# Performance work log

Hardware: AMD Instinct MI355X
Metric: run time of the kernel (lower is better)

## Reference

```python
import jax, jax.numpy as jnp
import numpy as np

IMAGE_SIZE = 512
N_ANGLES = 180
BATCH = 1


def setup_inputs() -> dict:
    key = jax.random.key(0)
    sinogram = jax.random.normal(key, (BATCH, N_ANGLES, IMAGE_SIZE), dtype=jnp.float32)
    angles = jnp.arange(N_ANGLES, dtype=jnp.float32)  # degrees, 0..179
    return {"sinogram": sinogram, "angles": angles}


def reference(sinogram, angles):
    # sinogram: [B, N, W]; returns [B, 1, H, W] with H == W == image_size.
    B, N, W = sinogram.shape
    H = W
    th = jnp.deg2rad(angles)
    c, s = jnp.cos(th)[:, None, None], jnp.sin(th)[:, None, None]  # [N,1,1]

    # affine_grid base coords (align_corners=True): linspace(-1, 1, size)
    xs = jnp.linspace(-1.0, 1.0, W)[None, None, :]  # [1,1,W]
    ys = jnp.linspace(-1.0, 1.0, H)[None, :, None]  # [1,H,1]

    # rotation: grid_x = c*x + s*y ; grid_y = -s*x + c*y   -> [N,H,W]
    gx = c * xs + s * ys
    gy = -s * xs + c * ys

    # unnormalize (align_corners=True)
    ix = (gx + 1.0) * 0.5 * (W - 1)
    iy = (gy + 1.0) * 0.5 * (H - 1)

    # bilinear corners in x (the input value only depends on the x index,
    # since the projection is expanded identically along H)
    x0 = jnp.floor(ix)
    x1 = x0 + 1.0
    wx1 = ix - x0
    wx0 = 1.0 - wx1
    mx0 = ((x0 >= 0) & (x0 <= W - 1)).astype(sinogram.dtype)
    mx1 = ((x1 >= 0) & (x1 <= W - 1)).astype(sinogram.dtype)
    x0i = jnp.clip(x0, 0, W - 1).astype(jnp.int32)
    x1i = jnp.clip(x1, 0, W - 1).astype(jnp.int32)

    # y contributes only a (zero-padding-masked) weight
    y0 = jnp.floor(iy)
    y1 = y0 + 1.0
    wy1 = iy - y0
    wy0 = 1.0 - wy1
    my0 = ((y0 >= 0) & (y0 <= H - 1)).astype(sinogram.dtype)
    my1 = ((y1 >= 0) & (y1 <= H - 1)).astype(sinogram.dtype)
    yw = wy0 * my0 + wy1 * my1  # [N,H,W]

    n_idx = jnp.arange(N)[:, None, None]  # [N,1,1]
    g0 = sinogram[:, n_idx, x0i]  # [B,N,H,W]
    g1 = sinogram[:, n_idx, x1i]  # [B,N,H,W]

    val = (wx0 * mx0 * g0 + wx1 * mx1 * g1) * yw  # [B,N,H,W]
    recon = jnp.sum(val, axis=1, keepdims=True) / N  # [B,1,H,W]
    return recon
```

## Files before the change

kernel.cpp:

```cpp
#include <hip/hip_runtime.h>
#include <hip/hip_bf16.h>
#include <math.h>


#define IRD_W 512
#define IRD_N 180
#define WIN   32
#define QN    45
#define IRD_STEP (2.0f / 511.0f)

__global__ __launch_bounds__(1024, 8) void iradon_tile4_kernel(
    const float* __restrict__ sino,
    const float* __restrict__ angles,
    float* __restrict__ out)
{
    __shared__ float4 s_c[IRD_N];
    __shared__ int2   s_base[IRD_N];
    __shared__ float  s_win[IRD_N][2 * WIN];
    __shared__ float  s_redA[3][256];
    __shared__ float  s_redB[3][256];

    const int tid = threadIdx.x;
    const int x0 = (blockIdx.x & 31) << 4;
    const int y0 = (blockIdx.x >> 5) << 4;
    const int b  = blockIdx.y;

    const float h = 255.5f;
    const float xs0 = -1.0f + (float)x0 * IRD_STEP;
    const float ys0 = -1.0f + (float)y0 * IRD_STEP;
    const float xs1 = xs0 + 15.0f * IRD_STEP;
    const float ys1 = ys0 + 15.0f * IRD_STEP;

    if (tid < IRD_N) {
        float th = angles[tid] * 0.017453292519943295f;
        float sv, cv;
        sincosf(th, &sv, &cv);
        const float ch = cv * h, sh = sv * h;
        const float cx0 = ch * xs0, cx1 = ch * xs1;
        const float sy0 = sh * ys0, sy1 = sh * ys1;
        const float minA = fminf(cx0, cx1) + fminf(sy0, sy1) + h;
        const float maxA = fmaxf(cx0, cx1) + fmaxf(sy0, sy1) + h;
        const int baseA = (int)floorf(minA) - 1;
        const int baseB = (int)floorf(511.0f - maxA) - 1;
        s_c[tid] = make_float4(ch, sh, h - (float)baseA,
                               (float)(511 - baseA - baseB));
        s_base[tid] = make_int2(baseA, baseB);
    }
    __syncthreads();

    const float* __restrict__ sb = sino + (size_t)b * (IRD_N * IRD_W);
    for (int idx = tid; idx < IRD_N * 2 * WIN; idx += 1024) {
        const int n    = idx >> 6;
        const int slot = idx & 63;
        const int base = (slot < WIN) ? s_base[n].x : s_base[n].y;
        const int src  = base + (slot & (WIN - 1));
        float v = 0.0f;
        if ((unsigned)src < IRD_W) v = sb[n * IRD_W + src];
        s_win[n][slot] = v;
    }
    __syncthreads();

    const int p = tid & 255;
    const int q = tid >> 8;
    const int x = x0 + (p & 15);
    const int y = y0 + (p >> 4);
    const float xs = -1.0f + (float)x * IRD_STEP;
    const float ys = -1.0f + (float)y * IRD_STEP;
    const float xsn = -xs;

    float accA = 0.0f, accB = 0.0f;

    const int n0 = q * QN;
    #pragma unroll 5
    for (int k = 0; k < QN; ++k) {
        const int n = n0 + k;
        const float4 t = s_c[n];
        const float ch = t.x, sh = t.y;

        const float ixr  = fmaf(ch, xs, fmaf(sh, ys, t.z));
        const float iy   = fmaf(ch, ys, fmaf(sh, xsn, h));
        const float ixmr = t.w - ixr;

        const float fA  = floorf(ixr);
        const float w1A = ixr - fA;
        const int   iA  = (int)fA;

        const float fB  = floorf(ixmr);
        const float w1B = ixmr - fB;
        const int   iB  = (int)fB;

        const float g0A = s_win[n][iA];
        const float g1A = s_win[n][iA + 1];
        const float g0B = s_win[n][WIN + iB];
        const float g1B = s_win[n][WIN + iB + 1];

        const float a  = __builtin_amdgcn_fmed3f(iy + 1.0f,   0.0f, 1.0f);
        const float bb = __builtin_amdgcn_fmed3f(512.0f - iy, 0.0f, 1.0f);
        const float yw = a * bb;

        accA = fmaf(fmaf(w1A, g1A - g0A, g0A), yw, accA);
        accB = fmaf(fmaf(w1B, g1B - g0B, g0B), yw, accB);
    }

    if (q != 0) {
        s_redA[q - 1][p] = accA;
        s_redB[q - 1][p] = accB;
    }
    __syncthreads();

    if (q == 0) {
        accA = ((accA + s_redA[0][p]) + s_redA[1][p]) + s_redA[2][p];
        accB = ((accB + s_redB[0][p]) + s_redB[1][p]) + s_redB[2][p];
        const int ob = b << 18;
        out[ob + (y << 9) + x]                 = accA * (1.0f / 180.0f);
        out[ob + ((511 - y) << 9) + (511 - x)] = accB * (1.0f / 180.0f);
    }
}

extern "C" void kernel_launch(void* const* d_in, const int* in_sizes, int n_in,
                              void* d_out, int out_size, void* d_ws, size_t ws_size,
                              hipStream_t stream) {
    const float* sino = (const float*)d_in[0];
    const float* angles = (const float*)d_in[1];
    float* out = (float*)d_out;

    const int B = out_size >> 18;
    dim3 grid(512, B > 0 ? B : 1);
    iradon_tile4_kernel<<<grid, 1024, 0, stream>>>(sino, angles, out);
}
```

Measured before the change: 20.43 us.

## Pack symmetric bilinear pairs as fp16 quads in one shared-memory load

Replaces the two separate per-tile sinogram windows with one window of packed half-precision quads. Each entry holds the two neighbouring samples for the pixel and the two mirrored samples for the point-symmetric pixel, so the inner loop does a single 8-byte LDS read instead of four scalar reads and computes only one floor. This cuts shared-memory traffic and ALU work per angle. Storing sinogram values in fp16 reduces accuracy, and reusing one index for the mirrored side depends on the exact symmetry of the sample positions.

```diff
diff --git a/kernel.cpp b/kernel.cpp
--- a/kernel.cpp
+++ b/kernel.cpp
@@ -1,5 +1,6 @@
 #include <hip/hip_runtime.h>
 #include <hip/hip_bf16.h>
+#include <hip/hip_fp16.h>
 #include <math.h>
 
 
@@ -9,14 +10,15 @@
 #define QN    45
 #define IRD_STEP (2.0f / 511.0f)
 
-__global__ __launch_bounds__(1024, 8) void iradon_tile4_kernel(
+__global__ __launch_bounds__(1024, 8) void iradon_quad_kernel(
     const float* __restrict__ sino,
     const float* __restrict__ angles,
     float* __restrict__ out)
 {
-    __shared__ float4 s_c[IRD_N];
-    __shared__ int2   s_base[IRD_N];
-    __shared__ float  s_win[IRD_N][2 * WIN];
+    __shared__ float2 s_cs[IRD_N];
+    __shared__ int    s_off[IRD_N];
+    __shared__ int    s_base[IRD_N];
+    __shared__ uint2  s_quad[IRD_N * WIN];
     __shared__ float  s_redA[3][256];
     __shared__ float  s_redB[3][256];
 
@@ -39,29 +41,33 @@
         const float cx0 = ch * xs0, cx1 = ch * xs1;
         const float sy0 = sh * ys0, sy1 = sh * ys1;
         const float minA = fminf(cx0, cx1) + fminf(sy0, sy1) + h;
-        const float maxA = fmaxf(cx0, cx1) + fmaxf(sy0, sy1) + h;
         const int baseA = (int)floorf(minA) - 1;
-        const int baseB = (int)floorf(511.0f - maxA) - 1;
-        s_c[tid] = make_float4(ch, sh, h - (float)baseA,
-                               (float)(511 - baseA - baseB));
-        s_base[tid] = make_int2(baseA, baseB);
+        s_cs[tid]  = make_float2(ch, sh);
+        s_off[tid] = (tid << 5) - baseA;
+        s_base[tid] = baseA;
     }
     __syncthreads();
 
     const float* __restrict__ sb = sino + (size_t)b * (IRD_N * IRD_W);
-    for (int idx = tid; idx < IRD_N * 2 * WIN; idx += 1024) {
-        const int n    = idx >> 6;
-        const int slot = idx & 63;
-        const int base = (slot < WIN) ? s_base[n].x : s_base[n].y;
-        const int src  = base + (slot & (WIN - 1));
-        float v = 0.0f;
-        if ((unsigned)src < IRD_W) v = sb[n * IRD_W + src];
-        s_win[n][slot] = v;
+    for (int idx = tid; idx < IRD_N * WIN; idx += 1024) {
+        const int n  = idx >> 5;
+        const int i  = idx & (WIN - 1);
+        const int gi = s_base[n] + i;
+        const float* __restrict__ row = sb + n * IRD_W;
+        const float g0 = ((unsigned)gi       < IRD_W) ? row[gi]       : 0.0f;
+        const float g1 = ((unsigned)(gi + 1) < IRD_W) ? row[gi + 1]   : 0.0f;
+        const float u  = ((unsigned)(510-gi) < IRD_W) ? row[510 - gi] : 0.0f;
+        const float v  = ((unsigned)(511-gi) < IRD_W) ? row[511 - gi] : 0.0f;
+        const __half2 hA  = __float22half2_rn(make_float2(g0, g1));
+        const __half2 hUV = __float22half2_rn(make_float2(u,  v));
+        s_quad[idx] = make_uint2(__builtin_bit_cast(unsigned, hA),
+                                 __builtin_bit_cast(unsigned, hUV));
     }
     __syncthreads();
 
     const int p = tid & 255;
     const int q = tid >> 8;
+    const int n0 = q * QN;
     const int x = x0 + (p & 15);
     const int y = y0 + (p >> 4);
     const float xs = -1.0f + (float)x * IRD_STEP;
@@ -70,36 +76,29 @@
 
     float accA = 0.0f, accB = 0.0f;
 
-    const int n0 = q * QN;
     #pragma unroll 5
     for (int k = 0; k < QN; ++k) {
         const int n = n0 + k;
-        const float4 t = s_c[n];
-        const float ch = t.x, sh = t.y;
+        const float2 cs = s_cs[n];
+        const int   off = s_off[n];
 
-        const float ixr  = fmaf(ch, xs, fmaf(sh, ys, t.z));
-        const float iy   = fmaf(ch, ys, fmaf(sh, xsn, h));
-        const float ixmr = t.w - ixr;
+        const float ix = fmaf(cs.x, xs, fmaf(cs.y, ys, h));
+        const float iy = fmaf(cs.x, ys, fmaf(cs.y, xsn, h));
 
-        const float fA  = floorf(ixr);
-        const float w1A = ixr - fA;
-        const int   iA  = (int)fA;
+        const float fg = floorf(ix);
+        const float w1 = ix - fg;
+        const int   gi = (int)fg;
 
-        const float fB  = floorf(ixmr);
-        const float w1B = ixmr - fB;
-        const int   iB  = (int)fB;
+        const uint2 q2 = s_quad[off + gi];
+        const float2 a  = __half22float2(__builtin_bit_cast(__half2, q2.x));
+        const float2 uv = __half22float2(__builtin_bit_cast(__half2, q2.y));
 
-        const float g0A = s_win[n][iA];
-        const float g1A = s_win[n][iA + 1];
-        const float g0B = s_win[n][WIN + iB];
-        const float g1B = s_win[n][WIN + iB + 1];
+        const float yw = __saturatef(iy + 1.0f) * __saturatef(512.0f - iy);
 
-        const float a  = __builtin_amdgcn_fmed3f(iy + 1.0f,   0.0f, 1.0f);
-        const float bb = __builtin_amdgcn_fmed3f(512.0f - iy, 0.0f, 1.0f);
-        const float yw = a * bb;
-
-        accA = fmaf(fmaf(w1A, g1A - g0A, g0A), yw, accA);
-        accB = fmaf(fmaf(w1B, g1B - g0B, g0B), yw, accB);
+        const float valA = fmaf(w1, a.y - a.x, a.x);
+        const float valB = fmaf(w1, uv.x - uv.y, uv.y);
+        accA = fmaf(valA, yw, accA);
+        accB = fmaf(valB, yw, accB);
     }
 
     if (q != 0) {
@@ -126,5 +125,5 @@
 
     const int B = out_size >> 18;
     dim3 grid(512, B > 0 ? B : 1);
-    iradon_tile4_kernel<<<grid, 1024, 0, stream>>>(sino, angles, out);
+    iradon_quad_kernel<<<grid, 1024, 0, stream>>>(sino, angles, out);
 }
```

New measurement: 24.28 us. 1.19x slower.

## Hoist angle sincos into prep kernel and use modular shared window indexing

Applied to the files above, without the earlier changes.

Moves the per-angle sincos computation into a separate tiny prep kernel that writes scaled cos/sin to workspace, so each of the 512 blocks no longer recomputes it. The shared-memory window is reorganised as a modulo-32 ring per angle, so one floor/fraction of the forward coordinate serves both the pixel and its point-mirrored pixel, with no separate base offsets. The inner loop therefore does one floor instead of two and reads cos/sin from global/cache instead of shared. It adds a second kernel launch and relies on the window fitting within 32 samples.

```diff
diff --git a/kernel.cpp b/kernel.cpp
--- a/kernel.cpp
+++ b/kernel.cpp
@@ -5,20 +5,30 @@
 
 #define IRD_W 512
 #define IRD_N 180
-#define WIN   32
 #define QN    45
+#define ROWW  68
 #define IRD_STEP (2.0f / 511.0f)
 
-__global__ __launch_bounds__(1024, 8) void iradon_tile4_kernel(
+__global__ void iradon_prep_kernel(const float* __restrict__ angles,
+                                   float2* __restrict__ cst) {
+    const int n = threadIdx.x;
+    if (n < IRD_N) {
+        float th = angles[n] * 0.017453292519943295f;
+        float sv, cv;
+        sincosf(th, &sv, &cv);
+        cst[n] = make_float2(cv * 255.5f, sv * 255.5f);
+    }
+}
+
+__global__ __launch_bounds__(1024, 8) void iradon_sg_kernel(
     const float* __restrict__ sino,
-    const float* __restrict__ angles,
+    const float2* __restrict__ cst,
     float* __restrict__ out)
 {
-    __shared__ float4 s_c[IRD_N];
-    __shared__ int2   s_base[IRD_N];
-    __shared__ float  s_win[IRD_N][2 * WIN];
-    __shared__ float  s_redA[3][256];
-    __shared__ float  s_redB[3][256];
+    __shared__ int2  s_base[IRD_N];
+    __shared__ float s_win[IRD_N][ROWW];
+    __shared__ float s_redA[3][256];
+    __shared__ float s_redB[3][256];
 
     const int tid = threadIdx.x;
     const int x0 = (blockIdx.x & 31) << 4;
@@ -32,74 +42,71 @@
     const float ys1 = ys0 + 15.0f * IRD_STEP;
 
     if (tid < IRD_N) {
-        float th = angles[tid] * 0.017453292519943295f;
-        float sv, cv;
-        sincosf(th, &sv, &cv);
-        const float ch = cv * h, sh = sv * h;
+        const float2 c = cst[tid];
+        const float ch = c.x, sh = c.y;
         const float cx0 = ch * xs0, cx1 = ch * xs1;
         const float sy0 = sh * ys0, sy1 = sh * ys1;
         const float minA = fminf(cx0, cx1) + fminf(sy0, sy1) + h;
         const float maxA = fmaxf(cx0, cx1) + fmaxf(sy0, sy1) + h;
         const int baseA = (int)floorf(minA) - 1;
         const int baseB = (int)floorf(511.0f - maxA) - 1;
-        s_c[tid] = make_float4(ch, sh, h - (float)baseA,
-                               (float)(511 - baseA - baseB));
         s_base[tid] = make_int2(baseA, baseB);
     }
     __syncthreads();
 
     const float* __restrict__ sb = sino + (size_t)b * (IRD_N * IRD_W);
-    for (int idx = tid; idx < IRD_N * 2 * WIN; idx += 1024) {
-        const int n    = idx >> 6;
-        const int slot = idx & 63;
-        const int base = (slot < WIN) ? s_base[n].x : s_base[n].y;
-        const int src  = base + (slot & (WIN - 1));
+    for (int t = tid; t < IRD_N * ROWW; t += 1024) {
+        const int n  = t / ROWW;
+        const int j  = t - n * ROWW;
+        const int2 bb = s_base[n];
+        const int isB  = j >= 34;
+        const int res  = (isB ? (j - 34) : j) & 31;
+        const int base = isB ? bb.y : bb.x;
+        const int src  = base + ((res - base) & 31);
         float v = 0.0f;
         if ((unsigned)src < IRD_W) v = sb[n * IRD_W + src];
-        s_win[n][slot] = v;
+        s_win[n][j] = v;
     }
     __syncthreads();
 
     const int p = tid & 255;
     const int q = tid >> 8;
+    const int n0 = q * QN;
     const int x = x0 + (p & 15);
     const int y = y0 + (p >> 4);
     const float xs = -1.0f + (float)x * IRD_STEP;
     const float ys = -1.0f + (float)y * IRD_STEP;
     const float xsn = -xs;
 
+    const float* __restrict__ wbase = &s_win[n0][0];
+    const float2* __restrict__ cq = cst + n0;
+
     float accA = 0.0f, accB = 0.0f;
 
-    const int n0 = q * QN;
     #pragma unroll 5
     for (int k = 0; k < QN; ++k) {
-        const int n = n0 + k;
-        const float4 t = s_c[n];
-        const float ch = t.x, sh = t.y;
+        const float2 c = cq[k];
+        const float ix = fmaf(c.x, xs, fmaf(c.y, ys, h));
+        const float iy = fmaf(c.x, ys, fmaf(c.y, xsn, h));
 
-        const float ixr  = fmaf(ch, xs, fmaf(sh, ys, t.z));
-        const float iy   = fmaf(ch, ys, fmaf(sh, xsn, h));
-        const float ixmr = t.w - ixr;
+        const float fg = floorf(ix);
+        const float w1 = ix - fg;
+        const int gi = (int)fg;
+        const int sA = gi & 31;
+        const int sB = (510 - gi) & 31;
 
-        const float fA  = floorf(ixr);
-        const float w1A = ixr - fA;
-        const int   iA  = (int)fA;
+        const float* __restrict__ rw = wbase + k * ROWW;
+        const float g0 = rw[sA];
+        const float g1 = rw[sA + 1];
+        const float u  = rw[34 + sB];
+        const float v  = rw[34 + sB + 1];
 
-        const float fB  = floorf(ixmr);
-        const float w1B = ixmr - fB;
-        const int   iB  = (int)fB;
+        const float a2 = __builtin_amdgcn_fmed3f(iy + 1.0f,   0.0f, 1.0f);
+        const float b2 = __builtin_amdgcn_fmed3f(512.0f - iy, 0.0f, 1.0f);
+        const float yw = a2 * b2;
 
-        const float g0A = s_win[n][iA];
-        const float g1A = s_win[n][iA + 1];
-        const float g0B = s_win[n][WIN + iB];
-        const float g1B = s_win[n][WIN + iB + 1];
-
-        const float a  = __builtin_amdgcn_fmed3f(iy + 1.0f,   0.0f, 1.0f);
-        const float bb = __builtin_amdgcn_fmed3f(512.0f - iy, 0.0f, 1.0f);
-        const float yw = a * bb;
-
-        accA = fmaf(fmaf(w1A, g1A - g0A, g0A), yw, accA);
-        accB = fmaf(fmaf(w1B, g1B - g0B, g0B), yw, accB);
+        accA = fmaf(fmaf(w1, g1 - g0, g0), yw, accA);
+        accB = fmaf(fmaf(w1, u - v,  v),  yw, accB);
     }
 
     if (q != 0) {
@@ -123,8 +130,11 @@
     const float* sino = (const float*)d_in[0];
     const float* angles = (const float*)d_in[1];
     float* out = (float*)d_out;
+    float2* cst = (float2*)d_ws;
+
+    iradon_prep_kernel<<<1, 256, 0, stream>>>(angles, cst);
 
     const int B = out_size >> 18;
     dim3 grid(512, B > 0 ? B : 1);
-    iradon_tile4_kernel<<<grid, 1024, 0, stream>>>(sino, angles, out);
+    iradon_sg_kernel<<<grid, 1024, 0, stream>>>(sino, cst, out);
 }
```

Measured after the change: 26.59 us. +30.2%, slower.
